# Kernel optimization log

Hardware: AMD Instinct MI355X
Metric: run time of the kernel (lower is better)

## Reference

```python
import jax, jax.numpy as jnp
import numpy as np

B, U1, U2 = 4, 2048, 2048
C = 256      # in_feat_dim
F = 256      # feat_dim
M = 4        # num_modes
D = C // M   # attention_mode_dim = 64
ATTN_CLIP = 500.0
LN_EPS = 1e-12


def setup_inputs() -> dict:
    key = jax.random.key(0)
    ks = jax.random.split(key, 8)
    s = 0.02  # base_initializer_range
    inp = {
        "query_feat": jax.random.normal(ks[0], (B, U1, C), jnp.float32),
        "key_feat": jax.random.normal(ks[1], (B, U2, C), jnp.float32),
        "Wq": jax.random.normal(ks[2], (M * D, C), jnp.float32) * s,
        "bq": jnp.zeros((M * D,), jnp.float32),
    }
    # tie_qk_scheme='shared': key linear shares query weights
    inp["Wk"] = inp["Wq"]
    inp["bk"] = inp["bq"]
    inp["Wv"] = jax.random.normal(ks[3], (M * F, C), jnp.float32) * s  # first_linear, v_has_bias=False
    inp["W_mid"] = jax.random.normal(ks[4], (F, F), jnp.float32) * s   # MMSharedMid shared_linear
    inp["b_mid"] = jnp.zeros((F,), jnp.float32)
    inp["W_out"] = jax.random.normal(ks[5], (M, F, F), jnp.float32) * s  # grouped 1x1 conv, per mode
    inp["b_out"] = jnp.zeros((M, F), jnp.float32)
    inp["ln_g"] = jnp.ones((F,), jnp.float32)   # resout LayerNorm
    inp["ln_b"] = jnp.zeros((F,), jnp.float32)
    inp["W_score"] = jax.random.normal(ks[6], (1, F), jnp.float32) * s  # LearnedSoftAggregate
    inp["b_score"] = jnp.zeros((1,), jnp.float32)
    return inp


def _layer_norm(x, g, b):
    mu = jnp.mean(x, axis=-1, keepdims=True)
    var = jnp.var(x, axis=-1, keepdims=True)
    return (x - mu) * jax.lax.rsqrt(var + LN_EPS) * g + b


def reference(query_feat, key_feat, Wq, bq, Wk, bk, Wv, W_mid, b_mid,
              W_out, b_out, ln_g, ln_b, W_score, b_score):
    # --- tied-QK multi-mode attention ---
    q = (query_feat @ Wq.T + bq).reshape(B, U1, M, D)
    k = (key_feat @ Wk.T + bk).reshape(B, U2, M, D)
    scores = jnp.einsum('bimd,bjmd->bmij', q, k) / jnp.sqrt(jnp.float32(D))
    scores = jnp.clip(scores, -ATTN_CLIP, ATTN_CLIP)  # attn_clip
    probs = jax.nn.softmax(scores, axis=-1)           # [B, M, U1, U2]

    # --- ExpandedFeatTrans: value projection + fusion ---
    v = (key_feat @ Wv.T).reshape(B, U2, M, F)        # first_linear (no bias)
    fused = jnp.einsum('bmij,bjmf->bmif', probs, v)   # [B, M, U1, F]

    # MMSharedMid: shared linear over F + gelu (dropout = identity in eval)
    mid = jax.nn.gelu(fused @ W_mid.T + b_mid, approximate=False)

    # MMPrivateOutput: per-mode grouped 1x1 conv; NOTE the original code computes
    # x_comb = x + shortcut but then layer-norms x (shortcut dropped) - kept faithful.
    out = jnp.einsum('bmif,mgf->bmig', mid, W_out) + b_out[None, :, None, :]
    out = _layer_norm(out, ln_g, ln_b)                # [B, M, U1, F]

    # LearnedSoftAggregate over modes (group_dim=1, keepdim=False)
    mode_scores = out @ W_score.T + b_score           # [B, M, U1, 1]
    mode_probs = jax.nn.softmax(mode_scores, axis=1)
    return jnp.sum(out * mode_probs, axis=1)          # [B, U1, F]
```

## Files before the change

kernel.cpp:

```cpp
#include <hip/hip_runtime.h>

typedef __attribute__((ext_vector_type(8))) short short8;
typedef __attribute__((ext_vector_type(4))) float f32x4;
typedef __attribute__((ext_vector_type(16))) float f32x16;
typedef __attribute__((ext_vector_type(4))) unsigned int u32x4;
typedef unsigned short u16t;
typedef unsigned int u32t;

#define MFMA16(a, b, c) __builtin_amdgcn_mfma_f32_16x16x32_bf16((a), (b), (c), 0, 0, 0)
#define MFMA32(a, b, c) __builtin_amdgcn_mfma_f32_32x32x16_bf16((a), (b), (c), 0, 0, 0)

__device__ __forceinline__ u16t f2bf(float f) {
  u32t u = __float_as_uint(f);
  u32t r = u + 0x7fffu + ((u >> 16) & 1u);
  return (u16t)(r >> 16);
}
__device__ __forceinline__ float bf2f(u16t b) {
  return __uint_as_float(((u32t)b) << 16);
}
__device__ __forceinline__ short8 pack8(float4 a0, float4 a1) {
  short8 r;
  r[0] = (short)f2bf(a0.x); r[1] = (short)f2bf(a0.y);
  r[2] = (short)f2bf(a0.z); r[3] = (short)f2bf(a0.w);
  r[4] = (short)f2bf(a1.x); r[5] = (short)f2bf(a1.y);
  r[6] = (short)f2bf(a1.z); r[7] = (short)f2bf(a1.w);
  return r;
}
__device__ __forceinline__ u32t packrhu(float a, float b) {
  u32t ua = __float_as_uint(a) + 0x8000u;
  u32t ub = __float_as_uint(b) + 0x8000u;
  return (ua >> 16) | (ub & 0xffff0000u);
}

__global__ void cvt_kernel(const float* __restrict__ src, u16t* __restrict__ dst, int n) {
  int i = blockIdx.x * 256 + threadIdx.x;
  if (i < n) dst[i] = f2bf(src[i]);
}

__global__ __launch_bounds__(256) void proj_gemm(
    const float* __restrict__ A, const float* __restrict__ W,
    const float* __restrict__ bias,
    u16t* __restrict__ out, int mode) {
  __shared__ __align__(16) u16t As[64 * 72];
  __shared__ __align__(16) u16t Ws[64 * 72];
  const int tid = threadIdx.x;
  const int w = tid >> 6, lane = tid & 63, quad = lane >> 4, l15 = lane & 15;
  const int l31 = lane & 31, h8 = (lane >> 5) * 8;
  const int rt = blockIdx.x * 64;
  const int ct = blockIdx.y * 64;
  const int wrow = (w >> 1) * 32, wcol = (w & 1) * 32;
  const int r2 = tid >> 3, c8 = tid & 7;

  const f32x4 fzero = {0.f, 0.f, 0.f, 0.f};
  f32x4 acc[2][2];
#pragma unroll
  for (int i = 0; i < 2; i++)
#pragma unroll
    for (int j = 0; j < 2; j++) acc[i][j] = fzero;

  for (int kt = 0; kt < 4; ++kt) {
    __syncthreads();
#pragma unroll
    for (int hh = 0; hh < 2; ++hh) {
      int rr = r2 + hh * 32;
      const float4* pa = (const float4*)(A + (size_t)(rt + rr) * 256 + kt * 64 + c8 * 8);
      const float4* pw = (const float4*)(W + (size_t)(ct + rr) * 256 + kt * 64 + c8 * 8);
      *(short8*)&As[rr * 72 + c8 * 8] = pack8(pa[0], pa[1]);
      *(short8*)&Ws[rr * 72 + c8 * 8] = pack8(pw[0], pw[1]);
    }
    __syncthreads();
#pragma unroll
    for (int ks = 0; ks < 2; ++ks) {
      short8 af0 = *(const short8*)&As[(wrow + l15) * 72 + ks * 32 + quad * 8];
      short8 af1 = *(const short8*)&As[(wrow + 16 + l15) * 72 + ks * 32 + quad * 8];
      short8 bw0 = *(const short8*)&Ws[(wcol + l15) * 72 + ks * 32 + quad * 8];
      short8 bw1 = *(const short8*)&Ws[(wcol + 16 + l15) * 72 + ks * 32 + quad * 8];
      acc[0][0] = MFMA16(af0, bw0, acc[0][0]);
      acc[0][1] = MFMA16(af0, bw1, acc[0][1]);
      acc[1][0] = MFMA16(af1, bw0, acc[1][0]);
      acc[1][1] = MFMA16(af1, bw1, acc[1][1]);
    }
  }

  __syncthreads();
  u16t* Cs = As;
  if (mode == 0) {
#pragma unroll
    for (int i = 0; i < 2; i++) {
      int rl = wrow + i * 16 + quad * 4;
#pragma unroll
      for (int j = 0; j < 2; j++) {
        int cl = wcol + j * 16 + l15;
        float bv = bias ? bias[ct + cl] : 0.f;
#pragma unroll
        for (int rg = 0; rg < 4; ++rg)
          Cs[(rl + rg) * 72 + cl] = f2bf(acc[i][j][rg] + bv);
      }
    }
  } else {
#pragma unroll
    for (int i = 0; i < 2; i++) {
      int rl = wrow + i * 16 + quad * 4;
#pragma unroll
      for (int j = 0; j < 2; j++) {
        int cl = wcol + j * 16 + l15;
        ushort4 pk;
        pk.x = f2bf(acc[i][j][0]);
        pk.y = f2bf(acc[i][j][1]);
        pk.z = f2bf(acc[i][j][2]);
        pk.w = f2bf(acc[i][j][3]);
        *(ushort4*)&Cs[cl * 72 + rl] = pk;
      }
    }
  }
  __syncthreads();

#pragma unroll
  for (int t2 = 0; t2 < 2; ++t2) {
    short8 frag = *(const short8*)&Cs[(t2 * 32 + l31) * 72 + w * 16 + h8];
    size_t base;
    if (mode == 0) {
      int b = rt >> 11, m = blockIdx.y;
      int it32 = ((rt & 2047) >> 5) + t2;
      base = (((size_t)(b * 4 + m) * 64 + it32) * 4 + w) * 512;
    } else {
      int b = rt >> 11, m = blockIdx.y >> 2;
      int fb = ((blockIdx.y & 3) << 1) + t2;
      int jt16 = ((rt & 2047) >> 4) + w;
      base = (((size_t)(b * 4 + m) * 8 + fb) * 128 + jt16) * 512;
    }
    *(short8*)(out + base + lane * 8) = frag;
  }
}

__global__ __launch_bounds__(256, 3) void attn_kernel(
    const u16t* __restrict__ Qf, const u16t* __restrict__ Kf,
    const u16t* __restrict__ Vf,
    const u16t* __restrict__ Wmid, const u16t* __restrict__ Wout,
    const float* __restrict__ b_mid, const float* __restrict__ b_out,
    const float* __restrict__ ln_g, const float* __restrict__ ln_b,
    const float* __restrict__ Wsc, const float* __restrict__ b_sc,
    u16t* __restrict__ out_ln, float* __restrict__ scoresWS) {
  __shared__ __align__(16) u16t smF[32 * 264];
  __shared__ float smR[128];
  __shared__ float smS[64];
  const int tid = threadIdx.x;
  const int w = tid >> 6, lane = tid & 63, quad = lane >> 4, l15 = lane & 15;
  const int l31 = lane & 31, h = lane >> 5;
  const int it32 = blockIdx.x;
  const int bm = blockIdx.y, m = bm & 3;
  const int q0 = it32 * 32;

  const size_t lane8 = (size_t)lane * 8;

  const u16t* qbase = Qf + ((size_t)(bm * 64 + it32) * 4) * 512 + lane8;
  short8 qf4[4];
#pragma unroll
  for (int ksd = 0; ksd < 4; ++ksd)
    qf4[ksd] = *(const short8*)(qbase + ksd * 512);

  const u16t* kbase = Kf + ((size_t)bm * 256) * 512 + lane8;
  const u16t* vbase = Vf + ((size_t)(bm * 8 + 2 * w) * 128) * 512 + lane8;

  f32x16 facc[2];
#pragma unroll
  for (int j = 0; j < 2; j++)
#pragma unroll
    for (int r = 0; r < 16; r++) facc[j][r] = 0.f;
  float lsum = 0.f;

#pragma unroll 1
  for (int jt = 0; jt < 64; ++jt) {
    short8 kf4[4];
#pragma unroll
    for (int ksd = 0; ksd < 4; ++ksd)
      kf4[ksd] = *(const short8*)(kbase + (size_t)jt * 2048 + ksd * 512);
    short8 vf4[2][2];
#pragma unroll
    for (int fb = 0; fb < 2; ++fb)
#pragma unroll
      for (int ks2 = 0; ks2 < 2; ++ks2)
        vf4[fb][ks2] = *(const short8*)(vbase + ((size_t)fb * 128 + 2 * jt + ks2) * 512);

    f32x16 sacc;
#pragma unroll
    for (int r = 0; r < 16; r++) sacc[r] = 0.f;
#pragma unroll
    for (int ksd = 0; ksd < 4; ++ksd)
      sacc = MFMA32(kf4[ksd], qf4[ksd], sacc);

    u32t pk[8];
    float ls = 0.f;
#pragma unroll
    for (int t = 0; t < 8; ++t) {
      float p0 = __expf(sacc[2 * t] * 0.125f);
      float p1 = __expf(sacc[2 * t + 1] * 0.125f);
      ls += p0 + p1;
      pk[t] = packrhu(p0, p1);
    }
    lsum += ls;

    u32t px[8];
#pragma unroll
    for (int t = 0; t < 8; ++t) px[t] = __shfl_xor(pk[t], 32);

    short8 bb[2];
#pragma unroll
    for (int ks2 = 0; ks2 < 2; ++ks2) {
      const int k4 = 4 * ks2;
      u32x4 bu;
      bu[0] = h ? px[k4 + 2] : pk[k4 + 0];
      bu[1] = h ? px[k4 + 3] : pk[k4 + 1];
      bu[2] = h ? pk[k4 + 2] : px[k4 + 0];
      bu[3] = h ? pk[k4 + 3] : px[k4 + 1];
      bb[ks2] = __builtin_bit_cast(short8, bu);
    }

    facc[0] = MFMA32(vf4[0][0], bb[0], facc[0]);
    facc[0] = MFMA32(vf4[0][1], bb[1], facc[0]);
    facc[1] = MFMA32(vf4[1][0], bb[0], facc[1]);
    facc[1] = MFMA32(vf4[1][1], bb[1], facc[1]);
  }

  lsum += __shfl_xor(lsum, 32);
  float inv = 1.f / lsum;

#pragma unroll
  for (int fb = 0; fb < 2; ++fb) {
#pragma unroll
    for (int g = 0; g < 4; ++g) {
      int fbase = w * 64 + fb * 32 + 8 * g + 4 * h;
      ushort4 pk4;
      pk4.x = f2bf(facc[fb][4 * g + 0] * inv);
      pk4.y = f2bf(facc[fb][4 * g + 1] * inv);
      pk4.z = f2bf(facc[fb][4 * g + 2] * inv);
      pk4.w = f2bf(facc[fb][4 * g + 3] * inv);
      *(ushort4*)&smF[l31 * 264 + fbase] = pk4;
    }
  }
  __syncthreads();

  const int rgrp = w >> 1, ch = w & 1;
  const int rowq = rgrp * 16 + quad * 4;
  const f32x4 fz4 = {0.f, 0.f, 0.f, 0.f};

  f32x4 macc[8];
#pragma unroll
  for (int i = 0; i < 8; i++) macc[i] = fz4;
  for (int kc = 0; kc < 8; ++kc) {
    short8 af = *(const short8*)&smF[(rgrp * 16 + l15) * 264 + kc * 32 + quad * 8];
#pragma unroll
    for (int nb = 0; nb < 8; ++nb) {
      short8 bw = *(const short8*)(Wmid + (size_t)(ch * 128 + nb * 16 + l15) * 256 + kc * 32 + quad * 8);
      macc[nb] = MFMA16(af, bw, macc[nb]);
    }
  }
#pragma unroll
  for (int nb = 0; nb < 8; ++nb) {
    int c = ch * 128 + nb * 16 + l15;
    float bmv = b_mid[c];
#pragma unroll
    for (int rg = 0; rg < 4; ++rg) {
      float x = macc[nb][rg] + bmv;
      macc[nb][rg] = 0.5f * x * (1.f + erff(x * 0.70710678118654752f));
    }
  }
  __syncthreads();
#pragma unroll
  for (int nb = 0; nb < 8; ++nb)
#pragma unroll
    for (int rg = 0; rg < 4; ++rg)
      smF[(rowq + rg) * 264 + ch * 128 + nb * 16 + l15] = f2bf(macc[nb][rg]);
  __syncthreads();

  const u16t* Wo = Wout + (size_t)m * 65536;
  f32x4 oacc[8];
#pragma unroll
  for (int i = 0; i < 8; i++) oacc[i] = fz4;
  for (int kc = 0; kc < 8; ++kc) {
    short8 af = *(const short8*)&smF[(rgrp * 16 + l15) * 264 + kc * 32 + quad * 8];
#pragma unroll
    for (int nb = 0; nb < 8; ++nb) {
      short8 bw = *(const short8*)(Wo + (size_t)(ch * 128 + nb * 16 + l15) * 256 + kc * 32 + quad * 8);
      oacc[nb] = MFMA16(af, bw, oacc[nb]);
    }
  }

  float sum[4] = {0, 0, 0, 0}, sq[4] = {0, 0, 0, 0};
#pragma unroll
  for (int nb = 0; nb < 8; ++nb) {
    int c = ch * 128 + nb * 16 + l15;
    float bo = b_out[m * 256 + c];
#pragma unroll
    for (int rg = 0; rg < 4; ++rg) {
      float x = oacc[nb][rg] + bo;
      oacc[nb][rg] = x;
      sum[rg] += x;
      sq[rg] += x * x;
    }
  }
#pragma unroll
  for (int rg = 0; rg < 4; ++rg) {
    float s = sum[rg], s2 = sq[rg];
    s += __shfl_xor(s, 1); s += __shfl_xor(s, 2); s += __shfl_xor(s, 4); s += __shfl_xor(s, 8);
    s2 += __shfl_xor(s2, 1); s2 += __shfl_xor(s2, 2); s2 += __shfl_xor(s2, 4); s2 += __shfl_xor(s2, 8);
    if (l15 == 0) {
      smR[(rowq + rg) + 32 * ch] = s;
      smR[64 + (rowq + rg) + 32 * ch] = s2;
    }
  }
  __syncthreads();
  float mu[4], rstd[4];
#pragma unroll
  for (int rg = 0; rg < 4; ++rg) {
    int r = rowq + rg;
    float s = smR[r] + smR[r + 32];
    float s2 = smR[64 + r] + smR[64 + r + 32];
    float mean = s * (1.f / 256.f);
    float var = s2 * (1.f / 256.f) - mean * mean;
    mu[rg] = mean;
    rstd[rg] = rsqrtf(var + 1e-12f);
  }

  float scp[4] = {0, 0, 0, 0};
#pragma unroll
  for (int nb = 0; nb < 8; ++nb) {
    int c = ch * 128 + nb * 16 + l15;
    float g = ln_g[c], bb2 = ln_b[c], wsv = Wsc[c];
#pragma unroll
    for (int rg = 0; rg < 4; ++rg) {
      float xn = (oacc[nb][rg] - mu[rg]) * rstd[rg] * g + bb2;
      out_ln[((size_t)bm * 2048 + (q0 + rowq + rg)) * 256 + c] = f2bf(xn);
      scp[rg] += xn * wsv;
    }
  }
#pragma unroll
  for (int rg = 0; rg < 4; ++rg) {
    float s = scp[rg];
    s += __shfl_xor(s, 1); s += __shfl_xor(s, 2); s += __shfl_xor(s, 4); s += __shfl_xor(s, 8);
    if (l15 == 0) smS[(rowq + rg) + 32 * ch] = s;
  }
  __syncthreads();
  if (ch == 0 && l15 == 0) {
#pragma unroll
    for (int rg = 0; rg < 4; ++rg) {
      int r = rowq + rg;
      scoresWS[bm * 2048 + q0 + r] = smS[r] + smS[r + 32] + b_sc[0];
    }
  }
}

__global__ __launch_bounds__(256) void agg_kernel(
    const u16t* __restrict__ out_ln, const float* __restrict__ scoresWS,
    float* __restrict__ out) {
  const int row = blockIdx.x;
  const int c = threadIdx.x;
  const int b = row >> 11, i = row & 2047;
  float s0 = scoresWS[(b * 4 + 0) * 2048 + i];
  float s1 = scoresWS[(b * 4 + 1) * 2048 + i];
  float s2 = scoresWS[(b * 4 + 2) * 2048 + i];
  float s3 = scoresWS[(b * 4 + 3) * 2048 + i];
  float mx = fmaxf(fmaxf(s0, s1), fmaxf(s2, s3));
  float e0 = __expf(s0 - mx), e1 = __expf(s1 - mx), e2 = __expf(s2 - mx), e3 = __expf(s3 - mx);
  float inv = 1.f / (e0 + e1 + e2 + e3);
  float acc = e0 * inv * bf2f(out_ln[((size_t)(b * 4 + 0) * 2048 + i) * 256 + c]) +
              e1 * inv * bf2f(out_ln[((size_t)(b * 4 + 1) * 2048 + i) * 256 + c]) +
              e2 * inv * bf2f(out_ln[((size_t)(b * 4 + 2) * 2048 + i) * 256 + c]) +
              e3 * inv * bf2f(out_ln[((size_t)(b * 4 + 3) * 2048 + i) * 256 + c]);
  out[(size_t)row * 256 + c] = acc;
}

extern "C" void kernel_launch(void* const* d_in, const int* in_sizes, int n_in,
                              void* d_out, int out_size, void* d_ws, size_t ws_size,
                              hipStream_t stream) {
  (void)in_sizes; (void)n_in; (void)out_size; (void)ws_size;
  const float* query = (const float*)d_in[0];
  const float* key   = (const float*)d_in[1];
  const float* Wq    = (const float*)d_in[2];
  const float* bq    = (const float*)d_in[3];
  const float* Wv    = (const float*)d_in[6];
  const float* Wm    = (const float*)d_in[7];
  const float* bmid  = (const float*)d_in[8];
  const float* Wo    = (const float*)d_in[9];
  const float* bo    = (const float*)d_in[10];
  const float* lng   = (const float*)d_in[11];
  const float* lnb   = (const float*)d_in[12];
  const float* Wsc   = (const float*)d_in[13];
  const float* bsc   = (const float*)d_in[14];

  char* p = (char*)d_ws;
  u16t* QfB = (u16t*)p; p += (size_t)2097152 * 2;
  u16t* KfB = (u16t*)p; p += (size_t)2097152 * 2;
  u16t* VfB = (u16t*)p; p += (size_t)8388608 * 2;
  u16t* WmB = (u16t*)p; p += (size_t)65536 * 2;
  u16t* WoB = (u16t*)p; p += (size_t)262144 * 2;
  u16t* outLn = (u16t*)p; p += (size_t)8388608 * 2;
  float* scWS = (float*)p; p += (size_t)32768 * 4;

  cvt_kernel<<<256, 256, 0, stream>>>(Wm, WmB, 65536);
  cvt_kernel<<<1024, 256, 0, stream>>>(Wo, WoB, 262144);

  proj_gemm<<<dim3(128, 4), 256, 0, stream>>>(query, Wq, bq, QfB, 0);
  proj_gemm<<<dim3(128, 4), 256, 0, stream>>>(key, Wq, bq, KfB, 0);
  proj_gemm<<<dim3(128, 16), 256, 0, stream>>>(key, Wv, nullptr, VfB, 1);

  attn_kernel<<<dim3(64, 16), 256, 0, stream>>>(QfB, KfB, VfB, WmB, WoB,
                                                bmid, bo, lng, lnb, Wsc, bsc,
                                                outLn, scWS);

  agg_kernel<<<8192, 256, 0, stream>>>(outLn, scWS, (float*)d_out);
}
```

Measured before the change: 277.7 us.

## Split QK score computation across waves and share probabilities through LDS

Previously every wave recomputed the full 32x32 QK^T score tile and exp for each key block, redundantly across 4 waves. Now each wave computes scores for a distinct 32-key slice, writes bf16 probabilities into a double-buffered LDS tile, and after a barrier all waves consume all four slices for their PV MFMAs. Row sums are combined across waves via shared memory at the end. This removes 4x redundant QK MFMA and exp work but adds a block barrier per iteration and LDS traffic.

```diff
diff --git a/kernel.cpp b/kernel.cpp
--- a/kernel.cpp
+++ b/kernel.cpp
@@ -3,7 +3,6 @@
 typedef __attribute__((ext_vector_type(8))) short short8;
 typedef __attribute__((ext_vector_type(4))) float f32x4;
 typedef __attribute__((ext_vector_type(16))) float f32x16;
-typedef __attribute__((ext_vector_type(4))) unsigned int u32x4;
 typedef unsigned short u16t;
 typedef unsigned int u32t;
 
@@ -142,6 +141,8 @@
     const float* __restrict__ Wsc, const float* __restrict__ b_sc,
     u16t* __restrict__ out_ln, float* __restrict__ scoresWS) {
   __shared__ __align__(16) u16t smF[32 * 264];
+  __shared__ __align__(16) u16t smP[2][32 * 132];
+  __shared__ float smL[128];
   __shared__ float smR[128];
   __shared__ float smS[64];
   const int tid = threadIdx.x;
@@ -170,17 +171,13 @@
   float lsum = 0.f;
 
 #pragma unroll 1
-  for (int jt = 0; jt < 64; ++jt) {
+  for (int t = 0; t < 16; ++t) {
+    u16t* Pb = &smP[t & 1][0];
+    const int jt32 = t * 4 + w;
     short8 kf4[4];
 #pragma unroll
     for (int ksd = 0; ksd < 4; ++ksd)
-      kf4[ksd] = *(const short8*)(kbase + (size_t)jt * 2048 + ksd * 512);
-    short8 vf4[2][2];
-#pragma unroll
-    for (int fb = 0; fb < 2; ++fb)
-#pragma unroll
-      for (int ks2 = 0; ks2 < 2; ++ks2)
-        vf4[fb][ks2] = *(const short8*)(vbase + ((size_t)fb * 128 + 2 * jt + ks2) * 512);
+      kf4[ksd] = *(const short8*)(kbase + (size_t)jt32 * 2048 + ksd * 512);
 
     f32x16 sacc;
 #pragma unroll
@@ -189,41 +186,42 @@
     for (int ksd = 0; ksd < 4; ++ksd)
       sacc = MFMA32(kf4[ksd], qf4[ksd], sacc);
 
-    u32t pk[8];
     float ls = 0.f;
 #pragma unroll
-    for (int t = 0; t < 8; ++t) {
-      float p0 = __expf(sacc[2 * t] * 0.125f);
-      float p1 = __expf(sacc[2 * t + 1] * 0.125f);
+    for (int tt = 0; tt < 8; ++tt) {
+      float p0 = __expf(sacc[2 * tt] * 0.125f);
+      float p1 = __expf(sacc[2 * tt + 1] * 0.125f);
       ls += p0 + p1;
-      pk[t] = packrhu(p0, p1);
+      const int jl = ((2 * tt) & 3) + 8 * ((2 * tt) >> 2) + 4 * h;
+      *(u32t*)&Pb[l31 * 132 + w * 32 + jl] = packrhu(p0, p1);
     }
     lsum += ls;
 
-    u32t px[8];
-#pragma unroll
-    for (int t = 0; t < 8; ++t) px[t] = __shfl_xor(pk[t], 32);
-
-    short8 bb[2];
-#pragma unroll
-    for (int ks2 = 0; ks2 < 2; ++ks2) {
-      const int k4 = 4 * ks2;
-      u32x4 bu;
-      bu[0] = h ? px[k4 + 2] : pk[k4 + 0];
-      bu[1] = h ? px[k4 + 3] : pk[k4 + 1];
-      bu[2] = h ? pk[k4 + 2] : px[k4 + 0];
-      bu[3] = h ? pk[k4 + 3] : px[k4 + 1];
-      bb[ks2] = __builtin_bit_cast(short8, bu);
-    }
-
-    facc[0] = MFMA32(vf4[0][0], bb[0], facc[0]);
-    facc[0] = MFMA32(vf4[0][1], bb[1], facc[0]);
-    facc[1] = MFMA32(vf4[1][0], bb[0], facc[1]);
-    facc[1] = MFMA32(vf4[1][1], bb[1], facc[1]);
+    __syncthreads();
+
+#pragma unroll
+    for (int jj = 0; jj < 4; ++jj) {
+      short8 vf[2][2];
+#pragma unroll
+      for (int fb = 0; fb < 2; ++fb)
+#pragma unroll
+        for (int ks2 = 0; ks2 < 2; ++ks2)
+          vf[fb][ks2] = *(const short8*)(vbase + ((size_t)fb * 128 + (t * 8 + jj * 2 + ks2)) * 512);
+      short8 bbL[2];
+#pragma unroll
+      for (int ks2 = 0; ks2 < 2; ++ks2)
+        bbL[ks2] = *(const short8*)&Pb[l31 * 132 + jj * 32 + ks2 * 16 + h * 8];
+      facc[0] = MFMA32(vf[0][0], bbL[0], facc[0]);
+      facc[0] = MFMA32(vf[0][1], bbL[1], facc[0]);
+      facc[1] = MFMA32(vf[1][0], bbL[0], facc[1]);
+      facc[1] = MFMA32(vf[1][1], bbL[1], facc[1]);
+    }
   }
 
   lsum += __shfl_xor(lsum, 32);
-  float inv = 1.f / lsum;
+  if (h == 0) smL[w * 32 + l31] = lsum;
+  __syncthreads();
+  float inv = 1.f / (smL[l31] + smL[32 + l31] + smL[64 + l31] + smL[96 + l31]);
 
 #pragma unroll
   for (int fb = 0; fb < 2; ++fb) {
```

Measured after the change: 252.1 us. 1.1x faster.
